# Kernel tuning notes

Hardware: AMD Instinct MI355X
Metric: run time of the kernel (lower is better)

The kernel has to match this reference:

```python
import jax, jax.numpy as jnp
import numpy as np

H = 1024          # hidden_size
E = 2 * H         # expansion e
S_DIM = 128       # shared q/k dim s
B, S = 4, 2048


def setup_inputs() -> dict:
    key = jax.random.key(0)
    ks = jax.random.split(key, 6)
    inputs = jax.random.normal(ks[0], (B, S, H), dtype=jnp.float32)
    W_uv = jax.random.normal(ks[1], (H, 2 * E + S_DIM), dtype=jnp.float32) * (1.0 / np.sqrt(H))
    b_uv = jnp.zeros((2 * E + S_DIM,), dtype=jnp.float32)
    gamma = jax.random.normal(ks[2], (2, S_DIM), dtype=jnp.float32) * 0.02
    beta = jnp.zeros((2, S_DIM), dtype=jnp.float32)
    W_out = jax.random.normal(ks[3], (E, H), dtype=jnp.float32) * (1.0 / np.sqrt(E))
    b_out = jnp.zeros((H,), dtype=jnp.float32)
    return {"inputs": inputs, "W_uv": W_uv, "b_uv": b_uv,
            "gamma": gamma, "beta": beta, "W_out": W_out, "b_out": b_out}


def reference(inputs, W_uv, b_uv, gamma, beta, W_out, b_out):
    seq_len = inputs.shape[1]
    # uv projection + SiLU
    uvb = jax.nn.silu(jnp.einsum('bsh,hf->bsf', inputs, W_uv) + b_uv)
    u = uvb[..., :E]                       # [B,S,E]
    v = uvb[..., E:2 * E]                  # [B,S,E]
    base = uvb[..., 2 * E:]                # [B,S,s]
    # per-head affine: [B,S,1,s]*[2,s] + [2,s] -> [B,S,2,s]
    qk = base[..., None, :] * gamma + beta
    q, k = qk[..., 0, :], qk[..., 1, :]    # [B,S,s] each
    scores = jnp.einsum('bns,bms->bnm', q, k) / seq_len   # [B,S,S]
    sq = jnp.square(jax.nn.relu(scores))
    attn_v = jnp.einsum('bnm,bme->bne', sq, v)            # [B,S,E]
    return jnp.einsum('bne,eh->bnh', u * attn_v, W_out) + b_out
```

## Files before the change

### kernel.cpp

```cpp
#include <hip/hip_runtime.h>
#include <stdint.h>


#define H_DIM  1024
#define E_DIM  2048
#define SD     128
#define B_SZ   4
#define S_LEN  2048
#define M_TOT  (B_SZ * S_LEN)
#define F_DIM  (2 * E_DIM + SD)

typedef _Float16 f16;
typedef __attribute__((ext_vector_type(4))) _Float16 f16x4;
typedef __attribute__((ext_vector_type(8))) _Float16 f16x8;
typedef __attribute__((ext_vector_type(16))) float f32x16;

__device__ __forceinline__ float silu_f(float x) { return x / (1.f + __expf(-x)); }

__device__ __forceinline__ void gload16(const void* g, void* l) {
  __builtin_amdgcn_global_load_lds(
      (const __attribute__((address_space(1))) void*)(uintptr_t)g,
      (__attribute__((address_space(3))) void*)(uint32_t)(uintptr_t)l,
      16, 0, 0);
}

__global__ __launch_bounds__(256) void cast_f16_k(const float* __restrict__ src,
                                                  f16* __restrict__ dst, long n) {
  long i = ((long)blockIdx.x * 256 + threadIdx.x) * 4;
  if (i < n) {
    float4 v = *(const float4*)(src + i);
    f16x4 h; h[0] = (f16)v.x; h[1] = (f16)v.y; h[2] = (f16)v.z; h[3] = (f16)v.w;
    *(f16x4*)(dst + i) = h;
  }
}

__global__ __launch_bounds__(256) void transpose_cast_k(const float* __restrict__ src,
                                                        f16* __restrict__ dst, int R, int C) {
  __shared__ float tile[32][33];
  int c0 = blockIdx.x * 32, r0 = blockIdx.y * 32;
  int tx = threadIdx.x & 31, ty = threadIdx.x >> 5;
  for (int i = ty; i < 32; i += 8) tile[i][tx] = src[(long)(r0 + i) * C + c0 + tx];
  __syncthreads();
  for (int i = ty; i < 32; i += 8) dst[(long)(c0 + i) * R + r0 + tx] = (f16)tile[tx][i];
}

template <int MODE>
__global__ __launch_bounds__(512, 2) void gemm256(
    const f16* __restrict__ Ag, const f16* __restrict__ Bg,
    float* __restrict__ F0, f16* __restrict__ O0, f16* __restrict__ O1,
    const f16* __restrict__ I0, const float* __restrict__ C0)
{
  constexpr int K  = (MODE == 0) ? H_DIM : 2048;
  constexpr int NT = K / 64;

  __shared__ f16 As[2][256][64];
  __shared__ f16 Bs[2][256][64];

  const int t    = threadIdx.x;
  const int w    = t >> 6;
  const int lane = t & 63;
  const int lo5  = lane & 31;
  const int hi   = lane >> 5;
  const int wm   = w >> 2;
  const int wn   = w & 3;

  const int gx  = gridDim.x;
  const int nwg = gx * gridDim.y;
  const int lin = blockIdx.y * gx + blockIdx.x;
  const int cpx = nwg >> 3;
  const int wg  = (lin & 7) * cpx + (lin >> 3);
  const int n0  = (wg % gx) * 256;
  const int m0  = (wg / gx) * 256;
  const long z  = blockIdx.z;

  const f16* A = Ag + (MODE == 2 ? z * (long)S_LEN * S_LEN : 0);
  const f16* B = Bg + (MODE == 2 ? z * (long)E_DIM * S_LEN : 0);

  auto stageA = [&](int bb, int half, int kt2) {
    const f16* g0 = A + (long)(m0 + half * 128) * K + kt2 * 64;
    f16* lb = &As[bb][half * 128][0];
#pragma unroll
    for (int j = 0; j < 2; j++) {
      int grp = (j << 3) + w;
      int rl  = (grp << 3) + (lane >> 3);
      gload16(g0 + (long)rl * K + (((lane & 7) ^ (lane >> 3) ^ (grp & 1)) << 3),
              lb + (grp << 9));
    }
  };
  auto stageB = [&](int bb, int half, int kt2) {
    const f16* g0 = B + (long)(n0 + half * 128) * K + kt2 * 64;
    f16* lb = &Bs[bb][half * 128][0];
#pragma unroll
    for (int j = 0; j < 2; j++) {
      int grp = (j << 3) + w;
      int rl  = (grp << 3) + (lane >> 3);
      gload16(g0 + (long)rl * K + (((lane & 7) ^ (lane >> 3) ^ (grp & 1)) << 3),
              lb + (grp << 9));
    }
  };

  f32x16 acc[4][2] = {};
  f16x8 a0[2][4], a1[2][4], b0[4], b1[4];

  const int swz = (lo5 & 7) ^ ((lo5 >> 3) & 1);
  const int rA  = wm * 64 + lo5;
  const int rB  = wn * 32 + lo5;

  stageA(0, 0, 0); stageA(0, 1, 0); stageB(0, 0, 0); stageB(0, 1, 0);
  stageA(1, 0, 1); stageA(1, 1, 1); stageB(1, 0, 1); stageB(1, 1, 1);
  asm volatile("s_waitcnt vmcnt(8)" ::: "memory");
  __builtin_amdgcn_s_barrier();

  for (int kt = 0; kt < NT; ++kt) {
    const int bf = kt & 1;
    const bool s2 = (kt + 2 < NT);

#pragma unroll
    for (int ksl = 0; ksl < 4; ksl++) {
      const int pc = ((((ksl << 1) + hi) ^ swz) << 3);
      a0[0][ksl] = *(const f16x8*)&As[bf][rA][pc];
      a0[1][ksl] = *(const f16x8*)&As[bf][rA + 32][pc];
      b0[ksl]    = *(const f16x8*)&Bs[bf][rB][pc];
    }
    __builtin_amdgcn_s_barrier();
    __builtin_amdgcn_s_setprio(1);
#pragma unroll
    for (int ksl = 0; ksl < 4; ksl++) {
      acc[0][0] = __builtin_amdgcn_mfma_f32_32x32x16_f16(a0[0][ksl], b0[ksl], acc[0][0], 0, 0, 0);
      acc[0][1] = __builtin_amdgcn_mfma_f32_32x32x16_f16(a0[1][ksl], b0[ksl], acc[0][1], 0, 0, 0);
    }
    __builtin_amdgcn_s_setprio(0);
    __builtin_amdgcn_s_barrier();

    if (s2) { stageA(bf, 0, kt + 2); stageB(bf, 0, kt + 2); }
#pragma unroll
    for (int ksl = 0; ksl < 4; ksl++) {
      const int pc = ((((ksl << 1) + hi) ^ swz) << 3);
      b1[ksl] = *(const f16x8*)&Bs[bf][128 + rB][pc];
    }
    __builtin_amdgcn_s_barrier();
    __builtin_amdgcn_s_setprio(1);
#pragma unroll
    for (int ksl = 0; ksl < 4; ksl++) {
      acc[1][0] = __builtin_amdgcn_mfma_f32_32x32x16_f16(a0[0][ksl], b1[ksl], acc[1][0], 0, 0, 0);
      acc[1][1] = __builtin_amdgcn_mfma_f32_32x32x16_f16(a0[1][ksl], b1[ksl], acc[1][1], 0, 0, 0);
    }
    __builtin_amdgcn_s_setprio(0);
    __builtin_amdgcn_s_barrier();

    if (s2) stageB(bf, 1, kt + 2);
#pragma unroll
    for (int ksl = 0; ksl < 4; ksl++) {
      const int pc = ((((ksl << 1) + hi) ^ swz) << 3);
      a1[0][ksl] = *(const f16x8*)&As[bf][128 + rA][pc];
      a1[1][ksl] = *(const f16x8*)&As[bf][128 + rA + 32][pc];
    }
    __builtin_amdgcn_s_barrier();
    __builtin_amdgcn_s_setprio(1);
#pragma unroll
    for (int ksl = 0; ksl < 4; ksl++) {
      acc[3][0] = __builtin_amdgcn_mfma_f32_32x32x16_f16(a1[0][ksl], b1[ksl], acc[3][0], 0, 0, 0);
      acc[3][1] = __builtin_amdgcn_mfma_f32_32x32x16_f16(a1[1][ksl], b1[ksl], acc[3][1], 0, 0, 0);
    }
    __builtin_amdgcn_s_setprio(0);
    __builtin_amdgcn_s_barrier();

    if (s2) stageA(bf, 1, kt + 2);
    __builtin_amdgcn_s_barrier();
    __builtin_amdgcn_s_setprio(1);
#pragma unroll
    for (int ksl = 0; ksl < 4; ksl++) {
      acc[2][0] = __builtin_amdgcn_mfma_f32_32x32x16_f16(a1[0][ksl], b0[ksl], acc[2][0], 0, 0, 0);
      acc[2][1] = __builtin_amdgcn_mfma_f32_32x32x16_f16(a1[1][ksl], b0[ksl], acc[2][1], 0, 0, 0);
    }
    __builtin_amdgcn_s_setprio(0);
    if (s2) { asm volatile("s_waitcnt vmcnt(8)" ::: "memory"); }
    else    { asm volatile("s_waitcnt vmcnt(0)" ::: "memory"); }
    __builtin_amdgcn_s_barrier();
  }

#pragma unroll
  for (int q = 0; q < 4; q++) {
    const int ms = q >> 1;
    const int ns = q & 1;
#pragma unroll
    for (int im = 0; im < 2; im++) {
      const int gc    = n0 + ns * 128 + wn * 32 + lo5;
      const int rbase = m0 + ms * 128 + wm * 64 + im * 32 + (hi << 2);
      if (MODE == 0) {
        const float bias = C0[gc];
        if (n0 < E_DIM) {
#pragma unroll
          for (int g = 0; g < 4; g++)
#pragma unroll
            for (int rr = 0; rr < 4; rr++) {
              int gr = rbase + (g << 3) + rr;
              O0[(long)gr * E_DIM + gc] = (f16)silu_f(acc[q][im][g * 4 + rr] + bias);
            }
        } else {
#pragma unroll
          for (int g = 0; g < 4; g++) {
            int gr0 = rbase + (g << 3);
            int b   = gr0 >> 11;
            int s0  = gr0 & (S_LEN - 1);
            f16x4 pk;
#pragma unroll
            for (int rr = 0; rr < 4; rr++) pk[rr] = (f16)silu_f(acc[q][im][g * 4 + rr] + bias);
            *(f16x4*)&O1[((long)b * E_DIM + (gc - E_DIM)) * S_LEN + s0] = pk;
          }
        }
      } else if (MODE == 2) {
        const long rowoff = z * S_LEN;
#pragma unroll
        for (int g = 0; g < 4; g++)
#pragma unroll
          for (int rr = 0; rr < 4; rr++) {
            int gr = rbase + (g << 3) + rr;
            long idx = (rowoff + gr) * (long)E_DIM + gc;
            O0[idx] = (f16)((float)I0[idx] * acc[q][im][g * 4 + rr]);
          }
      } else {
        const float bias = C0[gc];
#pragma unroll
        for (int g = 0; g < 4; g++)
#pragma unroll
          for (int rr = 0; rr < 4; rr++) {
            int gr = rbase + (g << 3) + rr;
            F0[(long)gr * H_DIM + gc] = acc[q][im][g * 4 + rr] * (1.0f / 17179869184.0f) + bias;
          }
      }
    }
  }
}

template <int MODE>
__global__ __launch_bounds__(256) void mfma_gemm(
    const f16* __restrict__ Ag, const f16* __restrict__ Bg,
    float* __restrict__ F0, f16* __restrict__ H0, const f16* __restrict__ H1,
    f16* __restrict__ H2, f16* __restrict__ H3,
    const float* __restrict__ C0, const float* __restrict__ C1,
    const float* __restrict__ C2)
{
  constexpr int K   = (MODE == 1) ? SD : H_DIM;
  constexpr int LDA = K, LDB = K;

  __shared__ f16 As[2][128][32];
  __shared__ f16 Bs[2][128][32];

  const int t    = threadIdx.x;
  const int w    = t >> 6;
  const int lane = t & 63;
  const int lo5  = lane & 31;
  const int hi   = lane >> 5;
  const int wy   = w >> 1, wx = w & 1;
  const int m0   = blockIdx.y * 128;
  const int n0   = blockIdx.x * 128;
  const long z   = blockIdx.z;

  const f16* A = Ag + (MODE == 1 ? z * (long)S_LEN * SD : 0);
  const f16* B = Bg + (MODE == 1 ? z * (long)S_LEN * SD : 0);

  const int srow = lane >> 2;
  const int scol = (((lane & 3) ^ ((srow >> 1) & 3))) * 8;
  const int rsw  = (lo5 >> 1) & 3;

  f32x16 acc[2][2] = {};

  for (int k0 = 0; k0 < K; k0 += 64) {
#pragma unroll
    for (int h = 0; h < 2; h++)
#pragma unroll
      for (int g16 = 0; g16 < 2; g16++) {
        const int r = (w << 5) + (g16 << 4);
        gload16(A + (long)(m0 + r + srow) * LDA + k0 + (h << 5) + scol, &As[h][r][0]);
        gload16(B + (long)(n0 + r + srow) * LDB + k0 + (h << 5) + scol, &Bs[h][r][0]);
      }
    __syncthreads();

#pragma unroll
    for (int ks = 0; ks < 4; ks++) {
      const int h  = ks >> 1;
      const int cl = ((ks & 1) << 1) + hi;
      const int kc = (cl ^ rsw) << 3;
      f16x8 av[2], bv[2];
#pragma unroll
      for (int i = 0; i < 2; i++)
        av[i] = *(const f16x8*)&As[h][(wy << 6) + (i << 5) + lo5][kc];
#pragma unroll
      for (int j = 0; j < 2; j++)
        bv[j] = *(const f16x8*)&Bs[h][(wx << 6) + (j << 5) + lo5][kc];
#pragma unroll
      for (int i = 0; i < 2; i++)
#pragma unroll
        for (int j = 0; j < 2; j++)
          acc[i][j] = __builtin_amdgcn_mfma_f32_32x32x16_f16(av[i], bv[j], acc[i][j], 0, 0, 0);
    }
    __syncthreads();
  }

  const int rb0 = m0 + (wy << 6) + (hi << 2);
  const int cb0 = n0 + (wx << 6) + lo5;

  if (MODE == 4) {
#pragma unroll
    for (int i = 0; i < 2; i++)
#pragma unroll
      for (int j = 0; j < 2; j++) {
        int jj = cb0 + (j << 5);
        float bias = C0[jj];
        float g0 = C1[jj], g1 = C1[SD + jj];
        float be0 = C2[jj], be1 = C2[SD + jj];
#pragma unroll
        for (int g = 0; g < 4; g++)
#pragma unroll
          for (int rr = 0; rr < 4; rr++) {
            int gr = rb0 + (i << 5) + (g << 3) + rr;
            float s = silu_f(acc[i][j][g * 4 + rr] + bias);
            H2[(long)gr * SD + jj] = (f16)(s * g0 + be0);
            H3[(long)gr * SD + jj] = (f16)(s * g1 + be1);
          }
      }
  } else {
#pragma unroll
    for (int i = 0; i < 2; i++)
#pragma unroll
      for (int j = 0; j < 2; j++) {
        int gc = cb0 + (j << 5);
#pragma unroll
        for (int g = 0; g < 4; g++)
#pragma unroll
          for (int rr = 0; rr < 4; rr++) {
            int gr = rb0 + (i << 5) + (g << 3) + rr;
            float tv = fmaxf(acc[i][j][g * 4 + rr], 0.f) * 64.f;
            H0[z * (long)S_LEN * S_LEN + (long)gr * S_LEN + gc] = (f16)(tv * tv);
          }
      }
  }
}

extern "C" void kernel_launch(void* const* d_in, const int* in_sizes, int n_in,
                              void* d_out, int out_size, void* d_ws, size_t ws_size,
                              hipStream_t stream) {
  const float* X     = (const float*)d_in[0];
  const float* W_uv  = (const float*)d_in[1];
  const float* b_uv  = (const float*)d_in[2];
  const float* gamma = (const float*)d_in[3];
  const float* beta  = (const float*)d_in[4];
  const float* W_out = (const float*)d_in[5];
  const float* b_out = (const float*)d_in[6];
  float* out = (float*)d_out;

  char* wp = (char*)d_ws;
  f16* Xh   = (f16*)wp; wp += (long)M_TOT * H_DIM * 2;
  f16* Wuvt = (f16*)wp; wp += (long)F_DIM * H_DIM * 2;
  f16* Wt   = (f16*)wp; wp += (long)H_DIM * E_DIM * 2;
  f16* u    = (f16*)wp; wp += (long)M_TOT * E_DIM * 2;
  f16* vt   = (f16*)wp; wp += (long)M_TOT * E_DIM * 2;
  f16* qh   = (f16*)wp; wp += (long)M_TOT * SD * 2;
  f16* kh   = (f16*)wp; wp += (long)M_TOT * SD * 2;
  f16* sq   = (f16*)wp; wp += (long)B_SZ * S_LEN * S_LEN * 2;
  f16* p    = (f16*)wp; wp += (long)M_TOT * E_DIM * 2;

  cast_f16_k<<<(M_TOT * H_DIM) / (256 * 4), 256, 0, stream>>>(X, Xh, (long)M_TOT * H_DIM);
  transpose_cast_k<<<dim3(F_DIM / 32, H_DIM / 32), 256, 0, stream>>>(W_uv, Wuvt, H_DIM, F_DIM);
  transpose_cast_k<<<dim3(H_DIM / 32, E_DIM / 32), 256, 0, stream>>>(W_out, Wt, E_DIM, H_DIM);

  gemm256<0><<<dim3(2 * E_DIM / 256, M_TOT / 256, 1), 512, 0, stream>>>(
      Xh, Wuvt, nullptr, u, vt, nullptr, b_uv);

  mfma_gemm<4><<<dim3(1, M_TOT / 128, 1), 256, 0, stream>>>(
      Xh, Wuvt + (long)2 * E_DIM * H_DIM, nullptr, nullptr, nullptr, qh, kh,
      b_uv + 2 * E_DIM, gamma, beta);

  mfma_gemm<1><<<dim3(S_LEN / 128, S_LEN / 128, B_SZ), 256, 0, stream>>>(
      qh, kh, nullptr, sq, nullptr, nullptr, nullptr, nullptr, nullptr, nullptr);

  gemm256<2><<<dim3(E_DIM / 256, S_LEN / 256, B_SZ), 512, 0, stream>>>(
      sq, vt, nullptr, p, nullptr, u, nullptr);

  gemm256<3><<<dim3(H_DIM / 256, M_TOT / 256, 1), 512, 0, stream>>>(
      p, Wt, out, nullptr, nullptr, nullptr, b_out);
}
```

Before: 371.3 us.

## Software-pipeline LDS fragment loads against MFMA quadrants in GEMM main loop

```diff
diff --git a/kernel.cpp b/kernel.cpp
--- a/kernel.cpp
+++ b/kernel.cpp
@@ -106,78 +106,84 @@
   const int rA  = wm * 64 + lo5;
   const int rB  = wn * 32 + lo5;
 
+  auto loadA0 = [&](int bb) {
+#pragma unroll
+    for (int k = 0; k < 4; k++) {
+      const int pc = ((((k << 1) + hi) ^ swz) << 3);
+      a0[0][k] = *(const f16x8*)&As[bb][rA][pc];
+      a0[1][k] = *(const f16x8*)&As[bb][rA + 32][pc];
+    }
+  };
+  auto loadA1 = [&](int bb) {
+#pragma unroll
+    for (int k = 0; k < 4; k++) {
+      const int pc = ((((k << 1) + hi) ^ swz) << 3);
+      a1[0][k] = *(const f16x8*)&As[bb][128 + rA][pc];
+      a1[1][k] = *(const f16x8*)&As[bb][128 + rA + 32][pc];
+    }
+  };
+  auto loadB0 = [&](int bb) {
+#pragma unroll
+    for (int k = 0; k < 4; k++) {
+      const int pc = ((((k << 1) + hi) ^ swz) << 3);
+      b0[k] = *(const f16x8*)&Bs[bb][rB][pc];
+    }
+  };
+  auto loadB1 = [&](int bb) {
+#pragma unroll
+    for (int k = 0; k < 4; k++) {
+      const int pc = ((((k << 1) + hi) ^ swz) << 3);
+      b1[k] = *(const f16x8*)&Bs[bb][128 + rB][pc];
+    }
+  };
+
+#define MMA(Q, AV, BV) do {                                                      \
+    __builtin_amdgcn_s_setprio(1);                                               \
+    _Pragma("unroll")                                                            \
+    for (int k_ = 0; k_ < 4; k_++) {                                             \
+      acc[Q][0] = __builtin_amdgcn_mfma_f32_32x32x16_f16(AV[0][k_], BV[k_],      \
+                                                         acc[Q][0], 0, 0, 0);    \
+      acc[Q][1] = __builtin_amdgcn_mfma_f32_32x32x16_f16(AV[1][k_], BV[k_],      \
+                                                         acc[Q][1], 0, 0, 0);    \
+    }                                                                            \
+    __builtin_amdgcn_s_setprio(0);                                               \
+  } while (0)
+
   stageA(0, 0, 0); stageA(0, 1, 0); stageB(0, 0, 0); stageB(0, 1, 0);
   stageA(1, 0, 1); stageA(1, 1, 1); stageB(1, 0, 1); stageB(1, 1, 1);
   asm volatile("s_waitcnt vmcnt(8)" ::: "memory");
   __builtin_amdgcn_s_barrier();
+  loadA0(0); loadB0(0);
 
   for (int kt = 0; kt < NT; ++kt) {
     const int bf = kt & 1;
-    const bool s2 = (kt + 2 < NT);
-
-#pragma unroll
-    for (int ksl = 0; ksl < 4; ksl++) {
-      const int pc = ((((ksl << 1) + hi) ^ swz) << 3);
-      a0[0][ksl] = *(const f16x8*)&As[bf][rA][pc];
-      a0[1][ksl] = *(const f16x8*)&As[bf][rA + 32][pc];
-      b0[ksl]    = *(const f16x8*)&Bs[bf][rB][pc];
-    }
+    const bool s2    = (kt + 2 < NT);
+    const bool lastt = (kt + 1 == NT);
+
+    loadA1(bf);
+    __builtin_amdgcn_sched_barrier(0);
+    MMA(0, a0, b0);
     __builtin_amdgcn_s_barrier();
-    __builtin_amdgcn_s_setprio(1);
-#pragma unroll
-    for (int ksl = 0; ksl < 4; ksl++) {
-      acc[0][0] = __builtin_amdgcn_mfma_f32_32x32x16_f16(a0[0][ksl], b0[ksl], acc[0][0], 0, 0, 0);
-      acc[0][1] = __builtin_amdgcn_mfma_f32_32x32x16_f16(a0[1][ksl], b0[ksl], acc[0][1], 0, 0, 0);
-    }
-    __builtin_amdgcn_s_setprio(0);
+
+    if (s2) { stageA(bf, 0, kt + 2); stageB(bf, 0, kt + 2); }
+    loadB1(bf);
+    __builtin_amdgcn_sched_barrier(0);
+    MMA(2, a1, b0);
     __builtin_amdgcn_s_barrier();
 
-    if (s2) { stageA(bf, 0, kt + 2); stageB(bf, 0, kt + 2); }
-#pragma unroll
-    for (int ksl = 0; ksl < 4; ksl++) {
-      const int pc = ((((ksl << 1) + hi) ^ swz) << 3);
-      b1[ksl] = *(const f16x8*)&Bs[bf][128 + rB][pc];
-    }
+    if (s2) stageA(bf, 1, kt + 2);
+    MMA(1, a0, b1);
     __builtin_amdgcn_s_barrier();
-    __builtin_amdgcn_s_setprio(1);
-#pragma unroll
-    for (int ksl = 0; ksl < 4; ksl++) {
-      acc[1][0] = __builtin_amdgcn_mfma_f32_32x32x16_f16(a0[0][ksl], b1[ksl], acc[1][0], 0, 0, 0);
-      acc[1][1] = __builtin_amdgcn_mfma_f32_32x32x16_f16(a0[1][ksl], b1[ksl], acc[1][1], 0, 0, 0);
-    }
-    __builtin_amdgcn_s_setprio(0);
-    __builtin_amdgcn_s_barrier();
 
     if (s2) stageB(bf, 1, kt + 2);
-#pragma unroll
-    for (int ksl = 0; ksl < 4; ksl++) {
-      const int pc = ((((ksl << 1) + hi) ^ swz) << 3);
-      a1[0][ksl] = *(const f16x8*)&As[bf][128 + rA][pc];
-      a1[1][ksl] = *(const f16x8*)&As[bf][128 + rA + 32][pc];
-    }
-    __builtin_amdgcn_s_barrier();
-    __builtin_amdgcn_s_setprio(1);
-#pragma unroll
-    for (int ksl = 0; ksl < 4; ksl++) {
-      acc[3][0] = __builtin_amdgcn_mfma_f32_32x32x16_f16(a1[0][ksl], b1[ksl], acc[3][0], 0, 0, 0);
-      acc[3][1] = __builtin_amdgcn_mfma_f32_32x32x16_f16(a1[1][ksl], b1[ksl], acc[3][1], 0, 0, 0);
-    }
-    __builtin_amdgcn_s_setprio(0);
-    __builtin_amdgcn_s_barrier();
-
-    if (s2) stageA(bf, 1, kt + 2);
-    __builtin_amdgcn_s_barrier();
-    __builtin_amdgcn_s_setprio(1);
-#pragma unroll
-    for (int ksl = 0; ksl < 4; ksl++) {
-      acc[2][0] = __builtin_amdgcn_mfma_f32_32x32x16_f16(a1[0][ksl], b0[ksl], acc[2][0], 0, 0, 0);
-      acc[2][1] = __builtin_amdgcn_mfma_f32_32x32x16_f16(a1[1][ksl], b0[ksl], acc[2][1], 0, 0, 0);
-    }
-    __builtin_amdgcn_s_setprio(0);
     if (s2) { asm volatile("s_waitcnt vmcnt(8)" ::: "memory"); }
     else    { asm volatile("s_waitcnt vmcnt(0)" ::: "memory"); }
     __builtin_amdgcn_s_barrier();
-  }
+    if (!lastt) { loadA0(bf ^ 1); loadB0(bf ^ 1); }
+    __builtin_amdgcn_sched_barrier(0);
+    MMA(3, a1, b1);
+  }
+#undef MMA
 
 #pragma unroll
   for (int q = 0; q < 4; q++) {
```

New measurement: 378.1 us. No clear change (+1.8%).
